# Kernel tuning notes

Measured on AMD Instinct MI355X. Metric: run time of the kernel, lower is better.

Reference implementation:

```python
import jax, jax.numpy as jnp
import numpy as np

B, L, D = 32, 256, 1024
H = 8
DQ = D // H            # 128, dim_q == dim_k
DS = 64                # dim_s
DM = 256               # dim_mlp_s
DF = 4096              # dim_feedforward
EPS = 1e-5


def _layernorm(x, g, b):
    mu = jnp.mean(x, axis=-1, keepdims=True)
    var = jnp.mean(jnp.square(x - mu), axis=-1, keepdims=True)
    return (x - mu) * jax.lax.rsqrt(var + EPS) * g + b


def setup_inputs() -> dict:
    key = jax.random.key(0)
    ks = jax.random.split(key, 20)
    s = 0.02
    inp = {
        'src': jax.random.normal(ks[0], (B, L, D), jnp.float32),
        'sf': jax.random.normal(ks[1], (B, DS), jnp.float32),
        'atten_mask': jax.random.randint(ks[2], (B, L, L), 0, 2, jnp.int32),
        # per-head projections, stacked over heads (in,out layout)
        'qw': jax.random.normal(ks[3], (H, D, DQ), jnp.float32) * s,
        'qb': jnp.zeros((H, DQ), jnp.float32),
        'kw': jax.random.normal(ks[4], (H, D, DQ), jnp.float32) * s,
        'kb': jnp.zeros((H, DQ), jnp.float32),
        'vw': jax.random.normal(ks[5], (H, D, DQ), jnp.float32) * s,
        'vb': jnp.zeros((H, DQ), jnp.float32),
        # per-head bias MLP: dim_s -> dim_mlp_s -> L*L
        'b1w': jax.random.normal(ks[6], (H, DS, DM), jnp.float32) * s,
        'b1b': jnp.zeros((H, DM), jnp.float32),
        'b2w': jax.random.normal(ks[7], (H, DM, L * L), jnp.float32) * s,
        'b2b': jnp.zeros((H, L * L), jnp.float32),
        # output projection
        'ow': jax.random.normal(ks[8], (H * DQ, D), jnp.float32) * s,
        'ob': jnp.zeros((D,), jnp.float32),
        # layernorms
        'ln1_g': jnp.ones((D,), jnp.float32), 'ln1_b': jnp.zeros((D,), jnp.float32),
        'ln2_g': jnp.ones((D,), jnp.float32), 'ln2_b': jnp.zeros((D,), jnp.float32),
        # feed-forward
        'w1': jax.random.normal(ks[9], (D, DF), jnp.float32) * s,
        'bf1': jnp.zeros((DF,), jnp.float32),
        'w2': jax.random.normal(ks[10], (DF, D), jnp.float32) * s,
        'bf2': jnp.zeros((D,), jnp.float32),
    }
    return inp


def reference(src, sf, atten_mask, qw, qb, kw, kb, vw, vb, b1w, b1b, b2w, b2b,
              ow, ob, ln1_g, ln1_b, ln2_g, ln2_b, w1, bf1, w2, bf2):
    mask = atten_mask.astype(bool)                      # (B,L,L)
    # per-head projections: (H,B,L,DQ)
    q = jnp.einsum('bld,hdq->hblq', src, qw) + qb[:, None, None, :]
    k = jnp.einsum('bld,hdq->hblq', src, kw) + kb[:, None, None, :]
    v = jnp.einsum('bld,hdq->hblq', src, vw) + vb[:, None, None, :]
    scale = q.shape[-1] ** 0.5
    scores = jnp.einsum('hblq,hbmq->hblm', q, k) / scale
    # masked_fill with constant 1e-9 (NOT -inf), as in the original
    scores = jnp.where(mask[None], jnp.float32(1e-9), scores)
    # per-head learned bias from side features, added AFTER softmax
    hid = jax.nn.relu(jnp.einsum('bs,hsm->hbm', sf, b1w) + b1b[:, None, :])
    bias = (jnp.einsum('hbm,hmn->hbn', hid, b2w) + b2b[:, None, :]).reshape(H, B, L, L)
    soft = jax.nn.softmax(scores, axis=-1) + bias
    out = jnp.einsum('hblm,hbmv->hblv', soft, v)        # (H,B,L,DQ)
    # faithful to original: each head's result is indexed [0] -> batch element 0
    head0 = out[:, 0]                                   # (H,L,DQ)
    hidden = jnp.transpose(head0, (1, 0, 2)).reshape(L, H * DQ)
    attn = hidden @ ow + ob                             # (L,D), broadcasts over batch
    x = _layernorm(src + attn[None], ln1_g, ln1_b)      # (B,L,D)
    ffn = jax.nn.relu(x @ w1 + bf1) @ w2 + bf2
    return _layernorm(x + ffn, ln2_g, ln2_b)
```

## Files before the change

kernel.cpp:

```cpp
#include <hip/hip_runtime.h>

typedef unsigned short u16;
typedef short s16x8 __attribute__((ext_vector_type(8)));
typedef u16 u16x4 __attribute__((ext_vector_type(4)));
typedef float f32x4 __attribute__((ext_vector_type(4)));

#define B_ 32
#define L_ 256
#define D_ 1024
#define H_ 8
#define DQ_ 128
#define DS_ 64
#define DM_ 256
#define DF_ 4096

__device__ __forceinline__ u16 f2bf(float f) {
  unsigned u = __float_as_uint(f);
  unsigned r = (u + 0x7FFFu + ((u >> 16) & 1u)) >> 16;
  return (u16)r;
}

__device__ __forceinline__ f32x4 mfma16(s16x8 a, s16x8 b, f32x4 c) {
  return __builtin_amdgcn_mfma_f32_16x16x32_bf16(a, b, c, 0, 0, 0);
}

#define GLDS16(g, l)                                                        \
  __builtin_amdgcn_global_load_lds(                                         \
      (__attribute__((address_space(1))) const void*)(g),                   \
      (__attribute__((address_space(3))) void*)(l), 16, 0, 0)

__global__ __launch_bounds__(256) void tconv(const float* __restrict__ in,
                                             u16* __restrict__ out, int K, int N,
                                             long sIn, long sOut) {
  __shared__ float t[32][33];
  const int tx = threadIdx.x & 31, ty = threadIdx.x >> 5;
  const long n0 = (long)blockIdx.x * 32, k0 = (long)blockIdx.y * 32;
  const float* ip = in + (long)blockIdx.z * sIn;
  u16* op = out + (long)blockIdx.z * sOut;
#pragma unroll
  for (int i = 0; i < 4; ++i)
    t[ty + i * 8][tx] = ip[(k0 + ty + i * 8) * N + n0 + tx];
  __syncthreads();
#pragma unroll
  for (int i = 0; i < 4; ++i)
    op[(n0 + ty + i * 8) * K + k0 + tx] = f2bf(t[tx][ty + i * 8]);
}

__global__ __launch_bounds__(256) void tconv_qkv(const float* __restrict__ qw,
                                                 const float* __restrict__ kw,
                                                 const float* __restrict__ vw,
                                                 u16* __restrict__ qwT,
                                                 u16* __restrict__ kwT,
                                                 u16* __restrict__ vwT) {
  __shared__ float t[32][33];
  const int tx = threadIdx.x & 31, ty = threadIdx.x >> 5;
  const long n0 = (long)blockIdx.x * 32, k0 = (long)blockIdx.y * 32;
  const int z = blockIdx.z, sel = z >> 3, h = z & 7;
  const float* ip = (sel == 0 ? qw : (sel == 1 ? kw : vw)) + (long)h * D_ * DQ_;
  u16* op = (sel == 0 ? qwT : (sel == 1 ? kwT : vwT)) + (long)h * DQ_ * D_;
#pragma unroll
  for (int i = 0; i < 4; ++i)
    t[ty + i * 8][tx] = ip[(k0 + ty + i * 8) * DQ_ + n0 + tx];
  __syncthreads();
#pragma unroll
  for (int i = 0; i < 4; ++i)
    op[(n0 + ty + i * 8) * D_ + k0 + tx] = f2bf(t[tx][ty + i * 8]);
}

__global__ __launch_bounds__(256) void conv_bf16(const float* __restrict__ in,
                                                 u16* __restrict__ out) {
  const int i = (blockIdx.x * 256 + threadIdx.x) * 4;
  float4 v = *(const float4*)(in + i);
  u16x4 o = {f2bf(v.x), f2bf(v.y), f2bf(v.z), f2bf(v.w)};
  *(u16x4*)(out + i) = o;
}

__global__ __launch_bounds__(256) void hid_kernel(
    const float* __restrict__ sf, const float* __restrict__ b1w,
    const float* __restrict__ b1b, float* __restrict__ nzv,
    int* __restrict__ nzi, int* __restrict__ nzcnt) {
  const int h = blockIdx.x;
  const int tid = threadIdx.x;
  __shared__ float s_sf[DS_];
  __shared__ int wcnt[4];
  if (tid < DS_) s_sf[tid] = sf[tid];
  __syncthreads();
  float a = b1b[h * DM_ + tid];
  const float* wp = b1w + (long)h * DS_ * DM_ + tid;
#pragma unroll 8
  for (int s = 0; s < DS_; ++s) a += s_sf[s] * wp[s * DM_];
  a = fmaxf(a, 0.f);
  const unsigned long long bal = __ballot(a > 0.f);
  const int lane = tid & 63, wv = tid >> 6;
  const int pc = __popcll(bal);
  if (lane == 0) wcnt[wv] = pc;
  __syncthreads();
  int base = 0;
  for (int i = 0; i < wv; ++i) base += wcnt[i];
  const int pos = base + __popcll(bal & ((1ull << lane) - 1ull));
  if (a > 0.f) { nzv[h * DM_ + pos] = a; nzi[h * DM_ + pos] = tid; }
  if (tid == 255) nzcnt[h] = base + pc;
}

__global__ __launch_bounds__(256) void bias_gemv(
    const float* __restrict__ nzv, const int* __restrict__ nzi,
    const int* __restrict__ nzcnt, const float* __restrict__ b2w,
    const float* __restrict__ b2b, float* __restrict__ biasb) {
  const int h = blockIdx.y;
  const int n0 = blockIdx.x * 1024;
  const int tid = threadIdx.x;
  __shared__ float sv[DM_];
  __shared__ int si[DM_];
  const int nnz = nzcnt[h];
  if (tid < DM_) { sv[tid] = nzv[h * DM_ + tid]; si[tid] = nzi[h * DM_ + tid]; }
  __syncthreads();
  const float* wb = b2w + (long)h * DM_ * 65536 + n0 + tid * 4;
  float4 acc = {0.f, 0.f, 0.f, 0.f};
  int j = 0;
  for (; j + 4 <= nnz; j += 4) {
    const float4 a0 = *(const float4*)(wb + (long)si[j] * 65536);
    const float4 a1 = *(const float4*)(wb + (long)si[j + 1] * 65536);
    const float4 a2 = *(const float4*)(wb + (long)si[j + 2] * 65536);
    const float4 a3 = *(const float4*)(wb + (long)si[j + 3] * 65536);
    const float v0 = sv[j], v1 = sv[j + 1], v2 = sv[j + 2], v3 = sv[j + 3];
    acc.x += v0 * a0.x + v1 * a1.x + v2 * a2.x + v3 * a3.x;
    acc.y += v0 * a0.y + v1 * a1.y + v2 * a2.y + v3 * a3.y;
    acc.z += v0 * a0.z + v1 * a1.z + v2 * a2.z + v3 * a3.z;
    acc.w += v0 * a0.w + v1 * a1.w + v2 * a2.w + v3 * a3.w;
  }
  for (; j < nnz; ++j) {
    const float4 a0 = *(const float4*)(wb + (long)si[j] * 65536);
    const float v0 = sv[j];
    acc.x += v0 * a0.x; acc.y += v0 * a0.y; acc.z += v0 * a0.z; acc.w += v0 * a0.w;
  }
  const float4 bb = *(const float4*)(b2b + (long)h * 65536 + n0 + tid * 4);
  float4 o = {acc.x + bb.x, acc.y + bb.y, acc.z + bb.z, acc.w + bb.w};
  *(float4*)(biasb + (long)h * 65536 + n0 + tid * 4) = o;
}

template <int EPI>
__global__ __launch_bounds__(256) void gemm_bt(
    const u16* __restrict__ A, const u16* __restrict__ BT, void* __restrict__ Cv,
    const float* __restrict__ bias, const float* __restrict__ R, int K, long sA,
    long sBT, long sC, long sBias, int ldc) {
  __shared__ u16 smA[128 * 32];
  __shared__ u16 smB[128 * 32];
  const int tid = threadIdx.x;
  const int lane = tid & 63;
  const int wv = tid >> 6;
  const int wr = wv >> 1, wc = wv & 1;
  const long tm = (long)blockIdx.x * 128;
  const long tn = (long)blockIdx.y * 128;
  const int z = blockIdx.z;
  A += (long)z * sA;
  BT += (long)z * sBT;

  const u16* ga = A + (tm + (tid >> 2)) * (long)K + (tid & 3) * 8;
  const u16* gb = BT + (tn + (tid >> 2)) * (long)K + (tid & 3) * 8;
  const long rstep = 64L * K;
  u16* la = &smA[tid * 8];
  u16* lb = &smB[tid * 8];

  f32x4 acc[4][4];
#pragma unroll
  for (int m = 0; m < 4; ++m)
#pragma unroll
    for (int n = 0; n < 4; ++n) acc[m][n] = (f32x4){0.f, 0.f, 0.f, 0.f};

  for (int k0 = 0; k0 < K; k0 += 32) {
    GLDS16(ga + k0, la);
    GLDS16(ga + rstep + k0, la + 64 * 32);
    GLDS16(gb + k0, lb);
    GLDS16(gb + rstep + k0, lb + 64 * 32);
    __syncthreads();
    s16x8 af[4], bf[4];
    const int ka = (lane >> 4) * 8;
    const int ra = wr * 64 + (lane & 15);
    const int rb = wc * 64 + (lane & 15);
#pragma unroll
    for (int m = 0; m < 4; ++m) af[m] = *(const s16x8*)&smA[(ra + m * 16) * 32 + ka];
#pragma unroll
    for (int n = 0; n < 4; ++n) bf[n] = *(const s16x8*)&smB[(rb + n * 16) * 32 + ka];
#pragma unroll
    for (int m = 0; m < 4; ++m)
#pragma unroll
      for (int n = 0; n < 4; ++n) acc[m][n] = mfma16(af[m], bf[n], acc[m][n]);
    __syncthreads();
  }

  const long crow0 = tm + wr * 64 + ((lane >> 4) * 4);
  const long ccol0 = tn + wc * 64 + (lane & 15);
#pragma unroll
  for (int m = 0; m < 4; ++m) {
#pragma unroll
    for (int n = 0; n < 4; ++n) {
#pragma unroll
      for (int i = 0; i < 4; ++i) {
        const long row = crow0 + m * 16 + i;
        const long col = ccol0 + n * 16;
        float v = acc[m][n][i] + bias[(long)z * sBias + col];
        if constexpr (EPI == 0) {
          ((float*)Cv)[(long)z * sC + row * ldc + col] = v;
        }
      }
    }
  }
}

__global__ __launch_bounds__(256) void qkv_gemm(
    const u16* __restrict__ src0b, const u16* __restrict__ qwT,
    const u16* __restrict__ kwT, const u16* __restrict__ vwT,
    const float* __restrict__ qb, const float* __restrict__ kb,
    const float* __restrict__ vb, u16* __restrict__ q0, u16* __restrict__ k0,
    u16* __restrict__ v0T) {
  __shared__ u16 smA[128 * 32];
  __shared__ u16 smB[128 * 32];
  const int tid = threadIdx.x;
  const int lane = tid & 63;
  const int wv = tid >> 6;
  const int wr = wv >> 1, wc = wv & 1;
  const long tm = (long)blockIdx.x * 128;
  const int z = blockIdx.z, sel = z >> 3, h = z & 7;
  const int K = D_;
  const u16* BT = (sel == 0 ? qwT : (sel == 1 ? kwT : vwT)) + (long)h * DQ_ * D_;
  const float* bias = (sel == 0 ? qb : (sel == 1 ? kb : vb)) + h * DQ_;

  const u16* ga = src0b + (tm + (tid >> 2)) * (long)K + (tid & 3) * 8;
  const u16* gb = BT + (long)(tid >> 2) * K + (tid & 3) * 8;
  const long rstep = 64L * K;
  u16* la = &smA[tid * 8];
  u16* lb = &smB[tid * 8];

  f32x4 acc[4][4];
#pragma unroll
  for (int m = 0; m < 4; ++m)
#pragma unroll
    for (int n = 0; n < 4; ++n) acc[m][n] = (f32x4){0.f, 0.f, 0.f, 0.f};

  for (int k0_ = 0; k0_ < K; k0_ += 32) {
    GLDS16(ga + k0_, la);
    GLDS16(ga + rstep + k0_, la + 64 * 32);
    GLDS16(gb + k0_, lb);
    GLDS16(gb + rstep + k0_, lb + 64 * 32);
    __syncthreads();
    s16x8 af[4], bf[4];
    const int ka = (lane >> 4) * 8;
    const int ra = wr * 64 + (lane & 15);
    const int rb = wc * 64 + (lane & 15);
#pragma unroll
    for (int m = 0; m < 4; ++m) af[m] = *(const s16x8*)&smA[(ra + m * 16) * 32 + ka];
#pragma unroll
    for (int n = 0; n < 4; ++n) bf[n] = *(const s16x8*)&smB[(rb + n * 16) * 32 + ka];
#pragma unroll
    for (int m = 0; m < 4; ++m)
#pragma unroll
      for (int n = 0; n < 4; ++n) acc[m][n] = mfma16(af[m], bf[n], acc[m][n]);
    __syncthreads();
  }

  const long crow0 = tm + wr * 64 + ((lane >> 4) * 4);
  const long ccol0 = wc * 64 + (lane & 15);
#pragma unroll
  for (int m = 0; m < 4; ++m) {
#pragma unroll
    for (int n = 0; n < 4; ++n) {
#pragma unroll
      for (int i = 0; i < 4; ++i) {
        const long row = crow0 + m * 16 + i;
        const long col = ccol0 + n * 16;
        const float v = acc[m][n][i] + bias[col];
        if (sel < 2) {
          u16* o = (sel == 0 ? q0 : k0) + (long)h * L_ * DQ_;
          o[row * DQ_ + col] = f2bf(v);
        } else {
          v0T[(long)h * DQ_ * L_ + col * L_ + row] = f2bf(v);
        }
      }
    }
  }
}

template <int BN, int EPI>
__global__ __launch_bounds__(512, 2) void gemm8p(
    const u16* __restrict__ A, const u16* __restrict__ BT, void* __restrict__ Cv,
    const float* __restrict__ bias, const float* __restrict__ R, int M, int N,
    int K, int ldc) {
  extern __shared__ char lds[];
  constexpr int NR = BN / 64;
  constexpr int NHB = BN / 128;
  constexpr int BUF = 32768 + BN * 128;
  constexpr int WST = (NHB == 2) ? 4 : 2;
  const int tid = threadIdx.x;
  const int lane = tid & 63;
  const int w = tid >> 6;
  const int wr = w >> 2, wc = w & 3;

  const int total = gridDim.x;
  int bid = blockIdx.x;
  int s = ((total & 7) == 0) ? ((bid & 7) * (total >> 3) + (bid >> 3)) : bid;
  const int gn = N / BN;
  const long tm = (long)(s / gn) * 256;
  const long tn = (long)(s % gn) * BN;
  const int NT = K >> 6;

  auto stageA = [&](int half, int t) {
    char* hb = lds + (long)(t & 1) * BUF + half * 16384;
    const u16* g = A + (tm + half * 128) * (long)K + (long)t * 64;
#pragma unroll
    for (int j = 0; j < 2; ++j) {
      const int idx = j * 512 + tid;
      const int r = idx >> 3;
      const int c16 = (idx & 7) ^ (r & 7);
      GLDS16(g + (long)r * K + c16 * 8, hb + idx * 16);
    }
  };
  auto stageB = [&](int half, int t) {
    char* hb = lds + (long)(t & 1) * BUF + 32768 + half * 16384;
    const u16* g = BT + (tn + half * 128) * (long)K + (long)t * 64;
#pragma unroll
    for (int j = 0; j < 2; ++j) {
      const int idx = j * 512 + tid;
      const int r = idx >> 3;
      const int c16 = (idx & 7) ^ (r & 7);
      GLDS16(g + (long)r * K + c16 * 8, hb + idx * 16);
    }
  };

  stageA(0, 0);
  stageA(1, 0);
  stageB(0, 0);
  if (NHB == 2) stageB(1, 0);
  stageB(0, 1);
  if (NHB == 2) stageB(1, 1);
  asm volatile("s_waitcnt vmcnt(%0)" ::"n"(WST) : "memory");
  __builtin_amdgcn_s_barrier();

  f32x4 acc[8][NR];
#pragma unroll
  for (int m = 0; m < 8; ++m)
#pragma unroll
    for (int n = 0; n < NR; ++n) acc[m][n] = (f32x4){0.f, 0.f, 0.f, 0.f};

  const int lk = (lane >> 4) * 16;
  const int lr = lane & 15;

  for (int t = 0; t < NT; ++t) {
    const char* bp = lds + (long)(t & 1) * BUF;
    s16x8 bfr[NR][2];
#pragma unroll
    for (int p = 0; p < 4; ++p) {
      if (p == 0) {
#pragma unroll
        for (int ni = 0; ni < NR; ++ni) {
          const int brow = wc * (BN / 4) + ni * 16 + lr;
#pragma unroll
          for (int ks = 0; ks < 2; ++ks) {
            const int kb = (ks * 64 + lk) ^ ((brow & 7) << 4);
            bfr[ni][ks] = *(const s16x8*)(bp + 32768 + brow * 128 + kb);
          }
        }
      }
      s16x8 afr[2][2];
#pragma unroll
      for (int rI = 0; rI < 2; ++rI) {
        const int arow = wr * 128 + (2 * p + rI) * 16 + lr;
#pragma unroll
        for (int ks = 0; ks < 2; ++ks) {
          const int kb = (ks * 64 + lk) ^ ((arow & 7) << 4);
          afr[rI][ks] = *(const s16x8*)(bp + arow * 128 + kb);
        }
      }
      if (p == 0) {
        if (t + 1 < NT) stageA(0, t + 1);
      } else if (p == 1) {
        if (t + 1 < NT) stageA(1, t + 1);
      } else if (p == 2) {
        if (t + 2 < NT) stageB(0, t + 2);
      } else {
        if (NHB == 2 && t + 2 < NT) stageB(1, t + 2);
      }
      __builtin_amdgcn_s_barrier();
      __builtin_amdgcn_s_setprio(1);
#pragma unroll
      for (int rI = 0; rI < 2; ++rI)
#pragma unroll
        for (int ni = 0; ni < NR; ++ni)
#pragma unroll
          for (int ks = 0; ks < 2; ++ks)
            acc[2 * p + rI][ni] = mfma16(afr[rI][ks], bfr[ni][ks], acc[2 * p + rI][ni]);
      __builtin_amdgcn_s_setprio(0);
      if (p == 3) {
        if (t + 2 < NT) {
          asm volatile("s_waitcnt vmcnt(%0)" ::"n"(WST) : "memory");
        } else if (t + 1 < NT) {
          asm volatile("s_waitcnt vmcnt(0)" ::: "memory");
        }
      }
      __builtin_amdgcn_s_barrier();
    }
  }

  const long crow0 = tm + wr * 128 + ((lane >> 4) * 4);
  const long ccol0 = tn + wc * (BN / 4) + lr;
#pragma unroll
  for (int m = 0; m < 8; ++m) {
#pragma unroll
    for (int n = 0; n < NR; ++n) {
#pragma unroll
      for (int i = 0; i < 4; ++i) {
        const long row = crow0 + m * 16 + i;
        const long col = ccol0 + n * 16;
        const float v = acc[m][n][i] + bias[col];
        if constexpr (EPI == 1) {
          ((u16*)Cv)[row * (long)ldc + col] = f2bf(fmaxf(v, 0.f));
        } else {
          ((float*)Cv)[row * (long)ldc + col] = v + R[row * (long)ldc + col];
        }
      }
    }
  }
}

__global__ __launch_bounds__(64) void attn_kernel(
    const u16* __restrict__ q0, const u16* __restrict__ k0,
    const u16* __restrict__ vT, const float* __restrict__ biasb,
    const int* __restrict__ mask0, u16* __restrict__ hidden) {
  const int lane = threadIdx.x;
  const int h = blockIdx.y;
  const int r0 = blockIdx.x * 16;
  const u16* q = q0 + (long)h * L_ * DQ_;
  const u16* k = k0 + (long)h * L_ * DQ_;
  const u16* v = vT + (long)h * DQ_ * L_;
  const int lg = lane >> 4;
  const int ll = lane & 15;

  s16x8 aq[4];
#pragma unroll
  for (int kk = 0; kk < 4; ++kk)
    aq[kk] = *(const s16x8*)(q + (long)(r0 + ll) * DQ_ + kk * 32 + lg * 8);

  float sc[16][4];
  const float scale = 0.08838834764831845f;
#pragma unroll
  for (int t = 0; t < 16; ++t) {
    f32x4 a = {0.f, 0.f, 0.f, 0.f};
#pragma unroll
    for (int kk = 0; kk < 4; ++kk) {
      s16x8 bf = *(const s16x8*)(k + (long)(t * 16 + ll) * DQ_ + kk * 32 + lg * 8);
      a = mfma16(aq[kk], bf, a);
    }
#pragma unroll
    for (int i = 0; i < 4; ++i) {
      const int row = r0 + lg * 4 + i;
      const int col = t * 16 + ll;
      float s = a[i] * scale;
      if (mask0[row * L_ + col] != 0) s = 1e-9f;
      sc[t][i] = s;
    }
  }
#pragma unroll
  for (int i = 0; i < 4; ++i) {
    float mx = sc[0][i];
#pragma unroll
    for (int t = 1; t < 16; ++t) mx = fmaxf(mx, sc[t][i]);
#pragma unroll
    for (int d = 1; d < 16; d <<= 1) mx = fmaxf(mx, __shfl_xor(mx, d));
    float sum = 0.f;
#pragma unroll
    for (int t = 0; t < 16; ++t) {
      const float e = __expf(sc[t][i] - mx);
      sc[t][i] = e;
      sum += e;
    }
#pragma unroll
    for (int d = 1; d < 16; d <<= 1) sum += __shfl_xor(sum, d);
    const float inv = 1.f / sum;
    const int row = r0 + lg * 4 + i;
#pragma unroll
    for (int t = 0; t < 16; ++t)
      sc[t][i] = sc[t][i] * inv + biasb[(long)h * 65536 + (long)row * 256 + t * 16 + ll];
  }
  __shared__ float sm[16 * 256];
#pragma unroll
  for (int t = 0; t < 16; ++t)
#pragma unroll
    for (int i = 0; i < 4; ++i)
      sm[(lg * 4 + i) * 256 + t * 16 + ll] = sc[t][i];
  __syncthreads();
  s16x8 af[8];
#pragma unroll
  for (int kk = 0; kk < 8; ++kk) {
    const float* ap = &sm[ll * 256 + kk * 32 + lg * 8];
    s16x8 t8;
#pragma unroll
    for (int j = 0; j < 8; ++j) t8[j] = (short)f2bf(ap[j]);
    af[kk] = t8;
  }
#pragma unroll
  for (int n = 0; n < 8; ++n) {
    f32x4 a = {0.f, 0.f, 0.f, 0.f};
#pragma unroll
    for (int kk = 0; kk < 8; ++kk) {
      s16x8 bf = *(const s16x8*)(v + (long)(n * 16 + ll) * 256 + kk * 32 + lg * 8);
      a = mfma16(af[kk], bf, a);
    }
#pragma unroll
    for (int i = 0; i < 4; ++i) {
      const int row = r0 + lg * 4 + i;
      const int col = n * 16 + ll;
      hidden[(long)row * 1024 + h * 128 + col] = f2bf(a[i]);
    }
  }
}

__global__ __launch_bounds__(256) void ln_kernel(
    const float* __restrict__ in0, const float* __restrict__ add1,
    const float* __restrict__ g, const float* __restrict__ bb,
    float* __restrict__ outf, u16* __restrict__ outb) {
  const int tid = threadIdx.x;
  const long row = blockIdx.x;
  float4 v = ((const float4*)(in0 + row * D_))[tid];
  if (add1) {
    const float4 u = ((const float4*)(add1 + (row & (L_ - 1)) * D_))[tid];
    v.x += u.x; v.y += u.y; v.z += u.z; v.w += u.w;
  }
  float s = v.x + v.y + v.z + v.w;
  float q = v.x * v.x + v.y * v.y + v.z * v.z + v.w * v.w;
#pragma unroll
  for (int d = 1; d < 64; d <<= 1) { s += __shfl_xor(s, d); q += __shfl_xor(q, d); }
  __shared__ float ss[4], sq[4];
  const int wv = tid >> 6;
  if ((tid & 63) == 0) { ss[wv] = s; sq[wv] = q; }
  __syncthreads();
  s = ss[0] + ss[1] + ss[2] + ss[3];
  q = sq[0] + sq[1] + sq[2] + sq[3];
  const float mu = s * (1.f / D_);
  const float var = q * (1.f / D_) - mu * mu;
  const float rs = rsqrtf(var + 1e-5f);
  const float4 gv = ((const float4*)g)[tid];
  const float4 bv = ((const float4*)bb)[tid];
  float4 o;
  o.x = (v.x - mu) * rs * gv.x + bv.x;
  o.y = (v.y - mu) * rs * gv.y + bv.y;
  o.z = (v.z - mu) * rs * gv.z + bv.z;
  o.w = (v.w - mu) * rs * gv.w + bv.w;
  ((float4*)(outf + row * D_))[tid] = o;
  if (outb) {
    uint2 pk;
    pk.x = (unsigned)f2bf(o.x) | ((unsigned)f2bf(o.y) << 16);
    pk.y = (unsigned)f2bf(o.z) | ((unsigned)f2bf(o.w) << 16);
    *(uint2*)(outb + row * D_ + tid * 4) = pk;
  }
}

extern "C" void kernel_launch(void* const* d_in, const int* in_sizes, int n_in,
                              void* d_out, int out_size, void* d_ws, size_t ws_size,
                              hipStream_t stream) {
  (void)in_sizes; (void)n_in; (void)out_size; (void)ws_size;
  const float* src = (const float*)d_in[0];
  const float* sf = (const float*)d_in[1];
  const int* mask = (const int*)d_in[2];
  const float* qw = (const float*)d_in[3];
  const float* qb = (const float*)d_in[4];
  const float* kw = (const float*)d_in[5];
  const float* kb = (const float*)d_in[6];
  const float* vw = (const float*)d_in[7];
  const float* vb = (const float*)d_in[8];
  const float* b1w = (const float*)d_in[9];
  const float* b1b = (const float*)d_in[10];
  const float* b2w = (const float*)d_in[11];
  const float* b2b = (const float*)d_in[12];
  const float* ow = (const float*)d_in[13];
  const float* ob = (const float*)d_in[14];
  const float* ln1g = (const float*)d_in[15];
  const float* ln1b = (const float*)d_in[16];
  const float* ln2g = (const float*)d_in[17];
  const float* ln2b = (const float*)d_in[18];
  const float* w1 = (const float*)d_in[19];
  const float* bf1 = (const float*)d_in[20];
  const float* w2 = (const float*)d_in[21];
  const float* bf2 = (const float*)d_in[22];
  float* out = (float*)d_out;

  char* ws = (char*)d_ws;
  size_t off = 0;
  auto alloc = [&](size_t bytes) {
    void* p = ws + off;
    off += (bytes + 255) & ~(size_t)255;
    return p;
  };
  u16* qwT = (u16*)alloc((size_t)H_ * DQ_ * D_ * 2);
  u16* kwT = (u16*)alloc((size_t)H_ * DQ_ * D_ * 2);
  u16* vwT = (u16*)alloc((size_t)H_ * DQ_ * D_ * 2);
  u16* owT = (u16*)alloc((size_t)D_ * D_ * 2);
  u16* w1T = (u16*)alloc((size_t)DF_ * D_ * 2);
  u16* w2T = (u16*)alloc((size_t)D_ * DF_ * 2);
  u16* src0b = (u16*)alloc((size_t)L_ * D_ * 2);
  u16* q0 = (u16*)alloc((size_t)H_ * L_ * DQ_ * 2);
  u16* k0 = (u16*)alloc((size_t)H_ * L_ * DQ_ * 2);
  u16* v0T = (u16*)alloc((size_t)H_ * DQ_ * L_ * 2);
  float* nzv = (float*)alloc((size_t)H_ * DM_ * 4);
  int* nzi = (int*)alloc((size_t)H_ * DM_ * 4);
  int* nzcnt = (int*)alloc(256);
  float* biasb = (float*)alloc((size_t)H_ * L_ * L_ * 4);
  u16* hidden = (u16*)alloc((size_t)L_ * H_ * DQ_ * 2);
  float* attnvec = (float*)alloc((size_t)L_ * D_ * 4);
  float* xf = (float*)alloc((size_t)B_ * L_ * D_ * 4);
  u16* xb = (u16*)alloc((size_t)B_ * L_ * D_ * 2);
  u16* ffnh = (u16*)alloc((size_t)B_ * L_ * DF_ * 2);

  hipFuncSetAttribute((const void*)gemm8p<256, 1>,
                      hipFuncAttributeMaxDynamicSharedMemorySize, 131072);
  hipFuncSetAttribute((const void*)gemm8p<128, 4>,
                      hipFuncAttributeMaxDynamicSharedMemorySize, 98304);

  const dim3 b256(256);
  tconv_qkv<<<dim3(DQ_ / 32, D_ / 32, 24), b256, 0, stream>>>(qw, kw, vw, qwT, kwT, vwT);
  tconv<<<dim3(D_ / 32, D_ / 32, 1), b256, 0, stream>>>(ow, owT, D_, D_, 0, 0);
  tconv<<<dim3(DF_ / 32, D_ / 32, 1), b256, 0, stream>>>(w1, w1T, D_, DF_, 0, 0);
  tconv<<<dim3(D_ / 32, DF_ / 32, 1), b256, 0, stream>>>(w2, w2T, DF_, D_, 0, 0);
  conv_bf16<<<dim3(L_ * D_ / 1024), b256, 0, stream>>>(src, src0b);

  hid_kernel<<<dim3(H_), b256, 0, stream>>>(sf, b1w, b1b, nzv, nzi, nzcnt);
  bias_gemv<<<dim3(64, H_), b256, 0, stream>>>(nzv, nzi, nzcnt, b2w, b2b, biasb);

  qkv_gemm<<<dim3(2, 1, 24), b256, 0, stream>>>(src0b, qwT, kwT, vwT, qb, kb, vb,
                                                q0, k0, v0T);

  attn_kernel<<<dim3(16, H_), dim3(64), 0, stream>>>(q0, k0, v0T, biasb, mask, hidden);

  gemm_bt<0><<<dim3(2, 8, 1), b256, 0, stream>>>(
      hidden, owT, attnvec, ob, nullptr, D_, 0, 0, 0, 0, D_);

  ln_kernel<<<dim3(B_ * L_), b256, 0, stream>>>(src, attnvec, ln1g, ln1b, xf, xb);

  gemm8p<256, 1><<<dim3(512), dim3(512), 131072, stream>>>(
      xb, w1T, ffnh, bf1, nullptr, B_ * L_, DF_, D_, DF_);
  gemm8p<128, 4><<<dim3(256), dim3(512), 98304, stream>>>(
      ffnh, w2T, xf, bf2, xf, B_ * L_, D_, DF_, D_);

  ln_kernel<<<dim3(B_ * L_), b256, 0, stream>>>(xf, nullptr, ln2g, ln2b, out, nullptr);
}
```

Baseline: 364.2 us.

## Merge prep kernels into two launches and keep residual stream in bf16

Folds the weight transposes, src conversion and hidden-MLP step into one prep kernel. The bias GEMV and the QKV GEMM are merged into a second kernel, which cuts launch count and lets these independent tasks share the GPU. The FFN residual and second-GEMM output are now bf16 (xb as residual, yb as output) instead of a separate fp32 xf buffer, so traffic in the down-projection epilogue and the final layernorm roughly halves. The cost is extra rounding of the residual sum to bf16 before the final layernorm, and the LN1 output is no longer stored in fp32.

```diff
diff --git a/kernel.cpp b/kernel.cpp
--- a/kernel.cpp
+++ b/kernel.cpp
@@ -19,6 +19,9 @@
   unsigned r = (u + 0x7FFFu + ((u >> 16) & 1u)) >> 16;
   return (u16)r;
 }
+__device__ __forceinline__ float bf2f(u16 x) {
+  return __uint_as_float(((unsigned)x) << 16);
+}
 
 __device__ __forceinline__ f32x4 mfma16(s16x8 a, s16x8 b, f32x4 c) {
   return __builtin_amdgcn_mfma_f32_16x16x32_bf16(a, b, c, 0, 0, 0);
@@ -29,120 +32,187 @@
       (__attribute__((address_space(1))) const void*)(g),                   \
       (__attribute__((address_space(3))) void*)(l), 16, 0, 0)
 
-__global__ __launch_bounds__(256) void tconv(const float* __restrict__ in,
-                                             u16* __restrict__ out, int K, int N,
-                                             long sIn, long sOut) {
+__device__ __forceinline__ void tile_tr(const float* __restrict__ ip,
+                                        u16* __restrict__ op, int K, int N,
+                                        int bx, int by, float (*t)[33], int tid) {
+  const int tx = tid & 31, ty = tid >> 5;
+  const long n0 = (long)bx * 32, k0 = (long)by * 32;
+#pragma unroll
+  for (int i = 0; i < 4; ++i)
+    t[ty + i * 8][tx] = ip[(k0 + ty + i * 8) * (long)N + n0 + tx];
+  __syncthreads();
+#pragma unroll
+  for (int i = 0; i < 4; ++i)
+    op[(n0 + ty + i * 8) * (long)K + k0 + tx] = f2bf(t[tx][ty + i * 8]);
+}
+
+__global__ __launch_bounds__(256) void prep(
+    const float* __restrict__ qw, const float* __restrict__ kw,
+    const float* __restrict__ vw, const float* __restrict__ ow,
+    const float* __restrict__ w1, const float* __restrict__ w2,
+    const float* __restrict__ src, const float* __restrict__ sf,
+    const float* __restrict__ b1w, const float* __restrict__ b1b,
+    u16* __restrict__ qwT, u16* __restrict__ kwT, u16* __restrict__ vwT,
+    u16* __restrict__ owT, u16* __restrict__ w1T, u16* __restrict__ w2T,
+    u16* __restrict__ src0b, float* __restrict__ nzv, int* __restrict__ nzi,
+    int* __restrict__ nzcnt) {
+  const int b = blockIdx.x;
+  const int tid = threadIdx.x;
   __shared__ float t[32][33];
-  const int tx = threadIdx.x & 31, ty = threadIdx.x >> 5;
-  const long n0 = (long)blockIdx.x * 32, k0 = (long)blockIdx.y * 32;
-  const float* ip = in + (long)blockIdx.z * sIn;
-  u16* op = out + (long)blockIdx.z * sOut;
-#pragma unroll
-  for (int i = 0; i < 4; ++i)
-    t[ty + i * 8][tx] = ip[(k0 + ty + i * 8) * N + n0 + tx];
-  __syncthreads();
-#pragma unroll
-  for (int i = 0; i < 4; ++i)
-    op[(n0 + ty + i * 8) * K + k0 + tx] = f2bf(t[tx][ty + i * 8]);
-}
-
-__global__ __launch_bounds__(256) void tconv_qkv(const float* __restrict__ qw,
-                                                 const float* __restrict__ kw,
-                                                 const float* __restrict__ vw,
-                                                 u16* __restrict__ qwT,
-                                                 u16* __restrict__ kwT,
-                                                 u16* __restrict__ vwT) {
-  __shared__ float t[32][33];
-  const int tx = threadIdx.x & 31, ty = threadIdx.x >> 5;
-  const long n0 = (long)blockIdx.x * 32, k0 = (long)blockIdx.y * 32;
-  const int z = blockIdx.z, sel = z >> 3, h = z & 7;
-  const float* ip = (sel == 0 ? qw : (sel == 1 ? kw : vw)) + (long)h * D_ * DQ_;
-  u16* op = (sel == 0 ? qwT : (sel == 1 ? kwT : vwT)) + (long)h * DQ_ * D_;
-#pragma unroll
-  for (int i = 0; i < 4; ++i)
-    t[ty + i * 8][tx] = ip[(k0 + ty + i * 8) * DQ_ + n0 + tx];
-  __syncthreads();
-#pragma unroll
-  for (int i = 0; i < 4; ++i)
-    op[(n0 + ty + i * 8) * D_ + k0 + tx] = f2bf(t[tx][ty + i * 8]);
-}
-
-__global__ __launch_bounds__(256) void conv_bf16(const float* __restrict__ in,
-                                                 u16* __restrict__ out) {
-  const int i = (blockIdx.x * 256 + threadIdx.x) * 4;
-  float4 v = *(const float4*)(in + i);
-  u16x4 o = {f2bf(v.x), f2bf(v.y), f2bf(v.z), f2bf(v.w)};
-  *(u16x4*)(out + i) = o;
-}
-
-__global__ __launch_bounds__(256) void hid_kernel(
-    const float* __restrict__ sf, const float* __restrict__ b1w,
-    const float* __restrict__ b1b, float* __restrict__ nzv,
-    int* __restrict__ nzi, int* __restrict__ nzcnt) {
-  const int h = blockIdx.x;
-  const int tid = threadIdx.x;
   __shared__ float s_sf[DS_];
   __shared__ int wcnt[4];
-  if (tid < DS_) s_sf[tid] = sf[tid];
-  __syncthreads();
-  float a = b1b[h * DM_ + tid];
-  const float* wp = b1w + (long)h * DS_ * DM_ + tid;
+  if (b < 3072) {
+    const int z = b >> 7, rem = b & 127;
+    const int sel = z >> 3, h = z & 7;
+    const float* ip = (sel == 0 ? qw : (sel == 1 ? kw : vw)) + (long)h * D_ * DQ_;
+    u16* op = (sel == 0 ? qwT : (sel == 1 ? kwT : vwT)) + (long)h * DQ_ * D_;
+    tile_tr(ip, op, D_, DQ_, rem & 3, rem >> 2, t, tid);
+  } else if (b < 4096) {
+    const int rem = b - 3072;
+    tile_tr(ow, owT, D_, D_, rem & 31, rem >> 5, t, tid);
+  } else if (b < 8192) {
+    const int rem = b - 4096;
+    tile_tr(w1, w1T, D_, DF_, rem & 127, rem >> 7, t, tid);
+  } else if (b < 12288) {
+    const int rem = b - 8192;
+    tile_tr(w2, w2T, DF_, D_, rem & 31, rem >> 5, t, tid);
+  } else if (b < 12544) {
+    const int rem = b - 12288;
+    const int i = (rem * 256 + tid) * 4;
+    float4 v = *(const float4*)(src + i);
+    u16x4 o = {f2bf(v.x), f2bf(v.y), f2bf(v.z), f2bf(v.w)};
+    *(u16x4*)(src0b + i) = o;
+  } else {
+    const int h = b - 12544;
+    if (tid < DS_) s_sf[tid] = sf[tid];
+    __syncthreads();
+    float a = b1b[h * DM_ + tid];
+    const float* wp = b1w + (long)h * DS_ * DM_ + tid;
 #pragma unroll 8
-  for (int s = 0; s < DS_; ++s) a += s_sf[s] * wp[s * DM_];
-  a = fmaxf(a, 0.f);
-  const unsigned long long bal = __ballot(a > 0.f);
-  const int lane = tid & 63, wv = tid >> 6;
-  const int pc = __popcll(bal);
-  if (lane == 0) wcnt[wv] = pc;
-  __syncthreads();
-  int base = 0;
-  for (int i = 0; i < wv; ++i) base += wcnt[i];
-  const int pos = base + __popcll(bal & ((1ull << lane) - 1ull));
-  if (a > 0.f) { nzv[h * DM_ + pos] = a; nzi[h * DM_ + pos] = tid; }
-  if (tid == 255) nzcnt[h] = base + pc;
-}
-
-__global__ __launch_bounds__(256) void bias_gemv(
+    for (int s = 0; s < DS_; ++s) a += s_sf[s] * wp[s * DM_];
+    a = fmaxf(a, 0.f);
+    const unsigned long long bal = __ballot(a > 0.f);
+    const int lane = tid & 63, wv = tid >> 6;
+    const int pc = __popcll(bal);
+    if (lane == 0) wcnt[wv] = pc;
+    __syncthreads();
+    int base = 0;
+    for (int i = 0; i < wv; ++i) base += wcnt[i];
+    const int pos = base + __popcll(bal & ((1ull << lane) - 1ull));
+    if (a > 0.f) { nzv[h * DM_ + pos] = a; nzi[h * DM_ + pos] = tid; }
+    if (tid == 255) nzcnt[h] = base + pc;
+  }
+}
+
+__global__ __launch_bounds__(256) void phase2(
     const float* __restrict__ nzv, const int* __restrict__ nzi,
     const int* __restrict__ nzcnt, const float* __restrict__ b2w,
-    const float* __restrict__ b2b, float* __restrict__ biasb) {
-  const int h = blockIdx.y;
-  const int n0 = blockIdx.x * 1024;
+    const float* __restrict__ b2b, float* __restrict__ biasb,
+    const u16* __restrict__ src0b, const u16* __restrict__ qwT,
+    const u16* __restrict__ kwT, const u16* __restrict__ vwT,
+    const float* __restrict__ qb, const float* __restrict__ kb,
+    const float* __restrict__ vb, u16* __restrict__ q0, u16* __restrict__ k0,
+    u16* __restrict__ v0T) {
+  const int b = blockIdx.x;
   const int tid = threadIdx.x;
   __shared__ float sv[DM_];
   __shared__ int si[DM_];
-  const int nnz = nzcnt[h];
-  if (tid < DM_) { sv[tid] = nzv[h * DM_ + tid]; si[tid] = nzi[h * DM_ + tid]; }
-  __syncthreads();
-  const float* wb = b2w + (long)h * DM_ * 65536 + n0 + tid * 4;
-  float4 acc = {0.f, 0.f, 0.f, 0.f};
-  int j = 0;
-  for (; j + 4 <= nnz; j += 4) {
-    const float4 a0 = *(const float4*)(wb + (long)si[j] * 65536);
-    const float4 a1 = *(const float4*)(wb + (long)si[j + 1] * 65536);
-    const float4 a2 = *(const float4*)(wb + (long)si[j + 2] * 65536);
-    const float4 a3 = *(const float4*)(wb + (long)si[j + 3] * 65536);
-    const float v0 = sv[j], v1 = sv[j + 1], v2 = sv[j + 2], v3 = sv[j + 3];
-    acc.x += v0 * a0.x + v1 * a1.x + v2 * a2.x + v3 * a3.x;
-    acc.y += v0 * a0.y + v1 * a1.y + v2 * a2.y + v3 * a3.y;
-    acc.z += v0 * a0.z + v1 * a1.z + v2 * a2.z + v3 * a3.z;
-    acc.w += v0 * a0.w + v1 * a1.w + v2 * a2.w + v3 * a3.w;
-  }
-  for (; j < nnz; ++j) {
-    const float4 a0 = *(const float4*)(wb + (long)si[j] * 65536);
-    const float v0 = sv[j];
-    acc.x += v0 * a0.x; acc.y += v0 * a0.y; acc.z += v0 * a0.z; acc.w += v0 * a0.w;
-  }
-  const float4 bb = *(const float4*)(b2b + (long)h * 65536 + n0 + tid * 4);
-  float4 o = {acc.x + bb.x, acc.y + bb.y, acc.z + bb.z, acc.w + bb.w};
-  *(float4*)(biasb + (long)h * 65536 + n0 + tid * 4) = o;
-}
-
-template <int EPI>
+  __shared__ u16 smA[128 * 32];
+  __shared__ u16 smB[128 * 32];
+  if (b < 512) {
+    const int h = b >> 6;
+    const int n0 = (b & 63) << 10;
+    const int nnz = nzcnt[h];
+    if (tid < DM_) { sv[tid] = nzv[h * DM_ + tid]; si[tid] = nzi[h * DM_ + tid]; }
+    __syncthreads();
+    const float* wb = b2w + (long)h * DM_ * 65536 + n0 + tid * 4;
+    float4 acc = {0.f, 0.f, 0.f, 0.f};
+    int j = 0;
+    for (; j + 4 <= nnz; j += 4) {
+      const float4 a0 = *(const float4*)(wb + (long)si[j] * 65536);
+      const float4 a1 = *(const float4*)(wb + (long)si[j + 1] * 65536);
+      const float4 a2 = *(const float4*)(wb + (long)si[j + 2] * 65536);
+      const float4 a3 = *(const float4*)(wb + (long)si[j + 3] * 65536);
+      const float v0 = sv[j], v1 = sv[j + 1], v2 = sv[j + 2], v3 = sv[j + 3];
+      acc.x += v0 * a0.x + v1 * a1.x + v2 * a2.x + v3 * a3.x;
+      acc.y += v0 * a0.y + v1 * a1.y + v2 * a2.y + v3 * a3.y;
+      acc.z += v0 * a0.z + v1 * a1.z + v2 * a2.z + v3 * a3.z;
+      acc.w += v0 * a0.w + v1 * a1.w + v2 * a2.w + v3 * a3.w;
+    }
+    for (; j < nnz; ++j) {
+      const float4 a0 = *(const float4*)(wb + (long)si[j] * 65536);
+      const float v0 = sv[j];
+      acc.x += v0 * a0.x; acc.y += v0 * a0.y; acc.z += v0 * a0.z; acc.w += v0 * a0.w;
+    }
+    const float4 bb = *(const float4*)(b2b + (long)h * 65536 + n0 + tid * 4);
+    float4 o = {acc.x + bb.x, acc.y + bb.y, acc.z + bb.z, acc.w + bb.w};
+    *(float4*)(biasb + (long)h * 65536 + n0 + tid * 4) = o;
+  } else {
+    const int r = b - 512;
+    const int z = r >> 1, sel = z >> 3, h = z & 7;
+    const long tm = (long)(r & 1) * 128;
+    const int K = D_;
+    const u16* BT = (sel == 0 ? qwT : (sel == 1 ? kwT : vwT)) + (long)h * DQ_ * D_;
+    const float* bias = (sel == 0 ? qb : (sel == 1 ? kb : vb)) + h * DQ_;
+    const int lane = tid & 63;
+    const int wv = tid >> 6;
+    const int wr = wv >> 1, wc = wv & 1;
+    const u16* ga = src0b + (tm + (tid >> 2)) * (long)K + (tid & 3) * 8;
+    const u16* gb = BT + (long)(tid >> 2) * K + (tid & 3) * 8;
+    const long rstep = 64L * K;
+    u16* la = &smA[tid * 8];
+    u16* lb = &smB[tid * 8];
+    f32x4 acc[4][4];
+#pragma unroll
+    for (int m = 0; m < 4; ++m)
+#pragma unroll
+      for (int n = 0; n < 4; ++n) acc[m][n] = (f32x4){0.f, 0.f, 0.f, 0.f};
+    for (int k0_ = 0; k0_ < K; k0_ += 32) {
+      GLDS16(ga + k0_, la);
+      GLDS16(ga + rstep + k0_, la + 64 * 32);
+      GLDS16(gb + k0_, lb);
+      GLDS16(gb + rstep + k0_, lb + 64 * 32);
+      __syncthreads();
+      s16x8 af[4], bf[4];
+      const int ka = (lane >> 4) * 8;
+      const int ra = wr * 64 + (lane & 15);
+      const int rb = wc * 64 + (lane & 15);
+#pragma unroll
+      for (int m = 0; m < 4; ++m) af[m] = *(const s16x8*)&smA[(ra + m * 16) * 32 + ka];
+#pragma unroll
+      for (int n = 0; n < 4; ++n) bf[n] = *(const s16x8*)&smB[(rb + n * 16) * 32 + ka];
+#pragma unroll
+      for (int m = 0; m < 4; ++m)
+#pragma unroll
+        for (int n = 0; n < 4; ++n) acc[m][n] = mfma16(af[m], bf[n], acc[m][n]);
+      __syncthreads();
+    }
+    const long crow0 = tm + wr * 64 + ((lane >> 4) * 4);
+    const long ccol0 = wc * 64 + (lane & 15);
+#pragma unroll
+    for (int m = 0; m < 4; ++m) {
+#pragma unroll
+      for (int n = 0; n < 4; ++n) {
+#pragma unroll
+        for (int i = 0; i < 4; ++i) {
+          const long row = crow0 + m * 16 + i;
+          const long col = ccol0 + n * 16;
+          const float v = acc[m][n][i] + bias[col];
+          if (sel < 2) {
+            u16* o = (sel == 0 ? q0 : k0) + (long)h * L_ * DQ_;
+            o[row * DQ_ + col] = f2bf(v);
+          } else {
+            v0T[(long)h * DQ_ * L_ + col * L_ + row] = f2bf(v);
+          }
+        }
+      }
+    }
+  }
+}
+
 __global__ __launch_bounds__(256) void gemm_bt(
-    const u16* __restrict__ A, const u16* __restrict__ BT, void* __restrict__ Cv,
-    const float* __restrict__ bias, const float* __restrict__ R, int K, long sA,
-    long sBT, long sC, long sBias, int ldc) {
+    const u16* __restrict__ A, const u16* __restrict__ BT, float* __restrict__ C,
+    const float* __restrict__ bias, int K, int ldc) {
   __shared__ u16 smA[128 * 32];
   __shared__ u16 smB[128 * 32];
   const int tid = threadIdx.x;
@@ -151,9 +221,6 @@
   const int wr = wv >> 1, wc = wv & 1;
   const long tm = (long)blockIdx.x * 128;
   const long tn = (long)blockIdx.y * 128;
-  const int z = blockIdx.z;
-  A += (long)z * sA;
-  BT += (long)z * sBT;
 
   const u16* ga = A + (tm + (tid >> 2)) * (long)K + (tid & 3) * 8;
   const u16* gb = BT + (tn + (tid >> 2)) * (long)K + (tid & 3) * 8;
@@ -191,99 +258,21 @@
   const long crow0 = tm + wr * 64 + ((lane >> 4) * 4);
   const long ccol0 = tn + wc * 64 + (lane & 15);
 #pragma unroll
-  for (int m = 0; m < 4; ++m) {
-#pragma unroll
-    for (int n = 0; n < 4; ++n) {
+  for (int m = 0; m < 4; ++m)
+#pragma unroll
+    for (int n = 0; n < 4; ++n)
 #pragma unroll
       for (int i = 0; i < 4; ++i) {
         const long row = crow0 + m * 16 + i;
         const long col = ccol0 + n * 16;
-        float v = acc[m][n][i] + bias[(long)z * sBias + col];
-        if constexpr (EPI == 0) {
-          ((float*)Cv)[(long)z * sC + row * ldc + col] = v;
-        }
+        C[row * (long)ldc + col] = acc[m][n][i] + bias[col];
       }
-    }
-  }
-}
-
-__global__ __launch_bounds__(256) void qkv_gemm(
-    const u16* __restrict__ src0b, const u16* __restrict__ qwT,
-    const u16* __restrict__ kwT, const u16* __restrict__ vwT,
-    const float* __restrict__ qb, const float* __restrict__ kb,
-    const float* __restrict__ vb, u16* __restrict__ q0, u16* __restrict__ k0,
-    u16* __restrict__ v0T) {
-  __shared__ u16 smA[128 * 32];
-  __shared__ u16 smB[128 * 32];
-  const int tid = threadIdx.x;
-  const int lane = tid & 63;
-  const int wv = tid >> 6;
-  const int wr = wv >> 1, wc = wv & 1;
-  const long tm = (long)blockIdx.x * 128;
-  const int z = blockIdx.z, sel = z >> 3, h = z & 7;
-  const int K = D_;
-  const u16* BT = (sel == 0 ? qwT : (sel == 1 ? kwT : vwT)) + (long)h * DQ_ * D_;
-  const float* bias = (sel == 0 ? qb : (sel == 1 ? kb : vb)) + h * DQ_;
-
-  const u16* ga = src0b + (tm + (tid >> 2)) * (long)K + (tid & 3) * 8;
-  const u16* gb = BT + (long)(tid >> 2) * K + (tid & 3) * 8;
-  const long rstep = 64L * K;
-  u16* la = &smA[tid * 8];
-  u16* lb = &smB[tid * 8];
-
-  f32x4 acc[4][4];
-#pragma unroll
-  for (int m = 0; m < 4; ++m)
-#pragma unroll
-    for (int n = 0; n < 4; ++n) acc[m][n] = (f32x4){0.f, 0.f, 0.f, 0.f};
-
-  for (int k0_ = 0; k0_ < K; k0_ += 32) {
-    GLDS16(ga + k0_, la);
-    GLDS16(ga + rstep + k0_, la + 64 * 32);
-    GLDS16(gb + k0_, lb);
-    GLDS16(gb + rstep + k0_, lb + 64 * 32);
-    __syncthreads();
-    s16x8 af[4], bf[4];
-    const int ka = (lane >> 4) * 8;
-    const int ra = wr * 64 + (lane & 15);
-    const int rb = wc * 64 + (lane & 15);
-#pragma unroll
-    for (int m = 0; m < 4; ++m) af[m] = *(const s16x8*)&smA[(ra + m * 16) * 32 + ka];
-#pragma unroll
-    for (int n = 0; n < 4; ++n) bf[n] = *(const s16x8*)&smB[(rb + n * 16) * 32 + ka];
-#pragma unroll
-    for (int m = 0; m < 4; ++m)
-#pragma unroll
-      for (int n = 0; n < 4; ++n) acc[m][n] = mfma16(af[m], bf[n], acc[m][n]);
-    __syncthreads();
-  }
-
-  const long crow0 = tm + wr * 64 + ((lane >> 4) * 4);
-  const long ccol0 = wc * 64 + (lane & 15);
-#pragma unroll
-  for (int m = 0; m < 4; ++m) {
-#pragma unroll
-    for (int n = 0; n < 4; ++n) {
-#pragma unroll
-      for (int i = 0; i < 4; ++i) {
-        const long row = crow0 + m * 16 + i;
-        const long col = ccol0 + n * 16;
-        const float v = acc[m][n][i] + bias[col];
-        if (sel < 2) {
-          u16* o = (sel == 0 ? q0 : k0) + (long)h * L_ * DQ_;
-          o[row * DQ_ + col] = f2bf(v);
-        } else {
-          v0T[(long)h * DQ_ * L_ + col * L_ + row] = f2bf(v);
-        }
-      }
-    }
-  }
 }
 
 template <int BN, int EPI>
 __global__ __launch_bounds__(512, 2) void gemm8p(
     const u16* __restrict__ A, const u16* __restrict__ BT, void* __restrict__ Cv,
-    const float* __restrict__ bias, const float* __restrict__ R, int M, int N,
+    const float* __restrict__ bias, const void* __restrict__ R, int M, int N,
     int K, int ldc) {
   extern __shared__ char lds[];
   constexpr int NR = BN / 64;
@@ -414,7 +403,8 @@
         if constexpr (EPI == 1) {
           ((u16*)Cv)[row * (long)ldc + col] = f2bf(fmaxf(v, 0.f));
         } else {
-          ((float*)Cv)[row * (long)ldc + col] = v + R[row * (long)ldc + col];
+          const float r = bf2f(((const u16*)R)[row * (long)ldc + col]);
+          ((u16*)Cv)[row * (long)ldc + col] = f2bf(v + r);
         }
       }
     }
@@ -513,16 +503,24 @@
   }
 }
 
+template <int MODE>
 __global__ __launch_bounds__(256) void ln_kernel(
-    const float* __restrict__ in0, const float* __restrict__ add1,
+    const void* __restrict__ in0v, const float* __restrict__ add1,
     const float* __restrict__ g, const float* __restrict__ bb,
-    float* __restrict__ outf, u16* __restrict__ outb) {
+    void* __restrict__ outv) {
   const int tid = threadIdx.x;
   const long row = blockIdx.x;
-  float4 v = ((const float4*)(in0 + row * D_))[tid];
-  if (add1) {
+  float4 v;
+  if constexpr (MODE == 0) {
+    v = ((const float4*)((const float*)in0v + row * D_))[tid];
     const float4 u = ((const float4*)(add1 + (row & (L_ - 1)) * D_))[tid];
     v.x += u.x; v.y += u.y; v.z += u.z; v.w += u.w;
+  } else {
+    const uint2 pk = *(const uint2*)((const u16*)in0v + row * D_ + tid * 4);
+    v.x = __uint_as_float((pk.x & 0xFFFFu) << 16);
+    v.y = __uint_as_float(pk.x & 0xFFFF0000u);
+    v.z = __uint_as_float((pk.y & 0xFFFFu) << 16);
+    v.w = __uint_as_float(pk.y & 0xFFFF0000u);
   }
   float s = v.x + v.y + v.z + v.w;
   float q = v.x * v.x + v.y * v.y + v.z * v.z + v.w * v.w;
@@ -544,12 +542,13 @@
   o.y = (v.y - mu) * rs * gv.y + bv.y;
   o.z = (v.z - mu) * rs * gv.z + bv.z;
   o.w = (v.w - mu) * rs * gv.w + bv.w;
-  ((float4*)(outf + row * D_))[tid] = o;
-  if (outb) {
+  if constexpr (MODE == 0) {
     uint2 pk;
     pk.x = (unsigned)f2bf(o.x) | ((unsigned)f2bf(o.y) << 16);
     pk.y = (unsigned)f2bf(o.z) | ((unsigned)f2bf(o.w) << 16);
-    *(uint2*)(outb + row * D_ + tid * 4) = pk;
+    *(uint2*)((u16*)outv + row * D_ + tid * 4) = pk;
+  } else {
+    ((float4*)((float*)outv + row * D_))[tid] = o;
   }
 }
 
@@ -605,39 +604,27 @@
   float* biasb = (float*)alloc((size_t)H_ * L_ * L_ * 4);
   u16* hidden = (u16*)alloc((size_t)L_ * H_ * DQ_ * 2);
   float* attnvec = (float*)alloc((size_t)L_ * D_ * 4);
-  float* xf = (float*)alloc((size_t)B_ * L_ * D_ * 4);
   u16* xb = (u16*)alloc((size_t)B_ * L_ * D_ * 2);
   u16* ffnh = (u16*)alloc((size_t)B_ * L_ * DF_ * 2);
+  u16* yb = (u16*)alloc((size_t)B_ * L_ * D_ * 2);
 
   hipFuncSetAttribute((const void*)gemm8p<256, 1>,
                       hipFuncAttributeMaxDynamicSharedMemorySize, 131072);
-  hipFuncSetAttribute((const void*)gemm8p<128, 4>,
+  hipFuncSetAttribute((const void*)gemm8p<128, 2>,
                       hipFuncAttributeMaxDynamicSharedMemorySize, 98304);
 
   const dim3 b256(256);
-  tconv_qkv<<<dim3(DQ_ / 32, D_ / 32, 24), b256, 0, stream>>>(qw, kw, vw, qwT, kwT, vwT);
-  tconv<<<dim3(D_ / 32, D_ / 32, 1), b256, 0, stream>>>(ow, owT, D_, D_, 0, 0);
-  tconv<<<dim3(DF_ / 32, D_ / 32, 1), b256, 0, stream>>>(w1, w1T, D_, DF_, 0, 0);
-  tconv<<<dim3(D_ / 32, DF_ / 32, 1), b256, 0, stream>>>(w2, w2T, DF_, D_, 0, 0);
-  conv_bf16<<<dim3(L_ * D_ / 1024), b256, 0, stream>>>(src, src0b);
-
-  hid_kernel<<<dim3(H_), b256, 0, stream>>>(sf, b1w, b1b, nzv, nzi, nzcnt);
-  bias_gemv<<<dim3(64, H_), b256, 0, stream>>>(nzv, nzi, nzcnt, b2w, b2b, biasb);
-
-  qkv_gemm<<<dim3(2, 1, 24), b256, 0, stream>>>(src0b, qwT, kwT, vwT, qb, kb, vb,
-                                                q0, k0, v0T);
-
+  prep<<<dim3(12552), b256, 0, stream>>>(qw, kw, vw, ow, w1, w2, src, sf, b1w, b1b,
+                                         qwT, kwT, vwT, owT, w1T, w2T, src0b, nzv,
+                                         nzi, nzcnt);
+  phase2<<<dim3(560), b256, 0, stream>>>(nzv, nzi, nzcnt, b2w, b2b, biasb, src0b,
+                                         qwT, kwT, vwT, qb, kb, vb, q0, k0, v0T);
   attn_kernel<<<dim3(16, H_), dim3(64), 0, stream>>>(q0, k0, v0T, biasb, mask, hidden);
-
-  gemm_bt<0><<<dim3(2, 8, 1), b256, 0, stream>>>(
-      hidden, owT, attnvec, ob, nullptr, D_, 0, 0, 0, 0, D_);
-
-  ln_kernel<<<dim3(B_ * L_), b256, 0, stream>>>(src, attnvec, ln1g, ln1b, xf, xb);
-
+  gemm_bt<<<dim3(2, 8), b256, 0, stream>>>(hidden, owT, attnvec, ob, D_, D_);
+  ln_kernel<0><<<dim3(B_ * L_), b256, 0, stream>>>(src, attnvec, ln1g, ln1b, xb);
   gemm8p<256, 1><<<dim3(512), dim3(512), 131072, stream>>>(
       xb, w1T, ffnh, bf1, nullptr, B_ * L_, DF_, D_, DF_);
-  gemm8p<128, 4><<<dim3(256), dim3(512), 98304, stream>>>(
-      ffnh, w2T, xf, bf2, xf, B_ * L_, D_, DF_, D_);
-
-  ln_kernel<<<dim3(B_ * L_), b256, 0, stream>>>(xf, nullptr, ln2g, ln2b, out, nullptr);
-}
+  gemm8p<128, 2><<<dim3(256), dim3(512), 98304, stream>>>(
+      ffnh, w2T, yb, bf2, xb, B_ * L_, D_, DF_, D_);
+  ln_kernel<1><<<dim3(B_ * L_), b256, 0, stream>>>(yb, nullptr, ln2g, ln2b, out);
+}
```

Result: faster. 329.0 us (-9.7%).
